# Optimization experiments

Hardware: AMD Instinct MI355X
Metric: run time of the kernel (lower is better)

The kernel has to match this reference:

```python
import jax, jax.numpy as jnp
import numpy as np

V, E, H, DV = 32000, 512, 1024, 512
B, K = 64, 49


def setup_inputs():
    key = jax.random.key(0)
    ks = jax.random.split(key, 16)
    p = lambda i, shape: jax.random.normal(ks[i], shape, dtype=jnp.float32) * 0.02
    return {
        "thought": jax.random.normal(ks[0], (B, H), dtype=jnp.float32),
        "visual_features": jax.random.normal(ks[1], (B, K, DV), dtype=jnp.float32),
        "max_len": 64,
        "embedding": p(2, (V, E)),
        "Wih1": p(3, (4 * H, E)), "Whh1": p(4, (4 * H, H)),
        "bih1": jnp.zeros((4 * H,), jnp.float32), "bhh1": jnp.zeros((4 * H,), jnp.float32),
        "Wih2": p(5, (4 * H, H)), "Whh2": p(6, (4 * H, H)),
        "bih2": jnp.zeros((4 * H,), jnp.float32), "bhh2": jnp.zeros((4 * H,), jnp.float32),
        "Wg1": p(7, (H, H)), "bg1": jnp.zeros((H,), jnp.float32),
        "Wg2": p(8, (1, H)), "bg2": jnp.zeros((1,), jnp.float32),
        "Wo": p(9, (V, H)), "bo": jnp.zeros((V,), jnp.float32),
        "Wv": p(10, (H, DV)), "bv": jnp.zeros((H,), jnp.float32),
        "ln_g": jnp.ones((H,), jnp.float32), "ln_b": jnp.zeros((H,), jnp.float32),
    }


def _lstm_cell(x, h, c, Wih, Whh, bih, bhh):
    # PyTorch LSTM gate order: i, f, g, o
    z = x @ Wih.T + h @ Whh.T + bih + bhh
    i, f, g, o = jnp.split(z, 4, axis=-1)
    c_new = jax.nn.sigmoid(f) * c + jax.nn.sigmoid(i) * jnp.tanh(g)
    h_new = jax.nn.sigmoid(o) * jnp.tanh(c_new)
    return h_new, c_new


def reference(thought, visual_features, max_len, embedding, Wih1, Whh1, bih1, bhh1,
              Wih2, Whh2, bih2, bbh2=None, bih2_dummy=None, **_unused):
    raise RuntimeError('placeholder')


def reference(thought, visual_features, max_len, embedding, Wih1, Whh1, bih1, bhh1,
              Wih2, Whh2, bih2, bhh2, Wg1, bg1, Wg2, bg2, Wo, bo, Wv, bv, ln_g, ln_b):
    Bsz, Hd = thought.shape
    temperature = 0.4  # epoch = 0 -> 0.4 + 0.4*0
    top_p = 0.7        # epoch = 0 -> 0.7 + 0.2*0
    scale = 1.0 / jnp.sqrt(jnp.asarray(Hd, jnp.float32))
    # visual_proj: Linear + LayerNorm (Dropout is identity in eval mode)
    vp = visual_features @ Wv.T + bv
    mu = vp.mean(-1, keepdims=True)
    var = vp.var(-1, keepdims=True)
    vp = (vp - mu) / jnp.sqrt(var + 1e-5) * ln_g + ln_b  # [B,K,H]
    b_idx = jnp.arange(Bsz)
    # carry: (h1,c1,h2,c2, input token, last-3 token history, history validity)
    init = (thought, jnp.zeros_like(thought), thought, jnp.zeros_like(thought),
            jnp.full((Bsz,), 1, jnp.int32),
            jnp.zeros((Bsz, 3), jnp.int32), jnp.zeros((Bsz, 3), jnp.bool_))
    keys = jax.random.split(jax.random.key(42), max_len)

    def step(carry, key):
        h1, c1, h2, c2, inp, hist, histv = carry
        emb = embedding[inp]  # [B,E]
        h1, c1 = _lstm_cell(emb, h1, c1, Wih1, Whh1, bih1, bhh1)
        h2, c2 = _lstm_cell(h1, h2, c2, Wih2, Whh2, bih2, bhh2)
        gate = jax.nn.sigmoid(jnp.tanh(h2 @ Wg1.T + bg1) @ Wg2.T + bg2)  # [B,1]
        out = h2 * gate
        attn = jax.nn.softmax(jnp.einsum('bh,bkh->bk', out, vp) * scale, axis=-1)
        out = out + jnp.einsum('bk,bkh->bh', attn, vp)
        logits = out @ Wo.T + bo  # [B,V]
        # repetition penalty: -2.0 once per UNIQUE token in last-3 history (set semantics via .max)
        pen = jnp.zeros_like(logits).at[b_idx[:, None], hist].max(histv.astype(logits.dtype))
        logits = (logits - 2.0 * pen) / temperature
        # nucleus (top-p) filtering, matching top_k_top_p_filtering with top_k=0
        order = jnp.argsort(-logits, axis=-1)
        sl = jnp.take_along_axis(logits, order, axis=-1)
        cum = jnp.cumsum(jax.nn.softmax(sl, axis=-1), axis=-1)
        rem = cum > top_p
        rem = jnp.concatenate([jnp.zeros_like(rem[:, :1]), rem[:, :-1]], axis=-1)
        mask = jnp.zeros_like(rem).at[b_idx[:, None], order].set(rem)
        logits = jnp.where(mask, -jnp.inf, logits)
        nxt = jax.random.categorical(key, logits).astype(jnp.int32)  # multinomial sample
        hist = jnp.concatenate([hist[:, 1:], nxt[:, None]], axis=1)
        histv = jnp.concatenate([histv[:, 1:], jnp.ones((Bsz, 1), jnp.bool_)], axis=1)
        return (h1, c1, h2, c2, nxt, hist, histv), nxt

    _, toks = jax.lax.scan(step, init, keys)
    return toks.T  # [B, max_len]
```

## Files before the change

### kernel.cpp

```cpp
#include <hip/hip_runtime.h>
#include <hip/hip_bf16.h>
#include <stdint.h>


#define B_   64
#define H_   1024
#define E_   512
#define DV_  512
#define KV_  49
#define V_   32000
#define T_   64

__device__ __forceinline__ uint32_t rotl32(uint32_t x, int r) {
  return (x << r) | (x >> (32 - r));
}
__device__ __forceinline__ void tf2x32(uint32_t k0, uint32_t k1,
                                       uint32_t x0, uint32_t x1,
                                       uint32_t& o0, uint32_t& o1) {
  uint32_t ks0 = k0, ks1 = k1, ks2 = k0 ^ k1 ^ 0x1BD11BDAu;
  x0 += ks0; x1 += ks1;
#define RND_(r) { x0 += x1; x1 = rotl32(x1, r) ^ x0; }
  RND_(13) RND_(15) RND_(26) RND_(6)  x0 += ks1; x1 += ks2 + 1u;
  RND_(17) RND_(29) RND_(16) RND_(24) x0 += ks2; x1 += ks0 + 2u;
  RND_(13) RND_(15) RND_(26) RND_(6)  x0 += ks0; x1 += ks1 + 3u;
  RND_(17) RND_(29) RND_(16) RND_(24) x0 += ks1; x1 += ks2 + 4u;
  RND_(13) RND_(15) RND_(26) RND_(6)  x0 += ks2; x1 += ks0 + 5u;
#undef RND_
  o0 = x0; o1 = x1;
}

__device__ __forceinline__ unsigned key_of(float f) {
  unsigned u = __float_as_uint(f);
  return (u & 0x80000000u) ? ~u : (u | 0x80000000u);
}
__device__ __forceinline__ float sigf(float x) { return 1.0f / (1.0f + expf(-x)); }

template <int BN, int TM, int TN, int NTHR>
__global__ __launch_bounds__(NTHR)
void gemm_dq(const float* __restrict__ A0, int lda0, const float* __restrict__ W0,
             int ldw0, int K0, float* __restrict__ out0, int ldo0, int nt0,
             const float* __restrict__ A1, int lda1, const float* __restrict__ W1,
             int ldw1, int K1, float* __restrict__ out1, int ldo1) {
  constexpr int LD = 36;
  constexpr int ROWS = 64 + BN;
  constexpr int NF4 = ROWS * 8 / NTHR;
  constexpr int BUFST = ROWS * LD;
  constexpr int CG = BN / TN;
  static_assert(ROWS * 8 % NTHR == 0, "staging divisibility");
  static_assert((64 / TM) * CG == NTHR, "thread grid");
  static_assert(TN == 4, "float4 epilogue");
  __shared__ __align__(16) float S[2][ROWS][LD];

  const int tid = threadIdx.x;
  const int bx = blockIdx.x;
  const float* A; const float* W; float* out;
  int lda, ldw, K, ldo, n0;
  if (bx < nt0) { A = A0; W = W0; out = out0; lda = lda0; ldw = ldw0; K = K0; ldo = ldo0; n0 = bx * BN; }
  else          { A = A1; W = W1; out = out1; lda = lda1; ldw = ldw1; K = K1; ldo = ldo1; n0 = (bx - nt0) * BN; }
  const int m0 = blockIdx.y * 64;
  const int tc = tid % CG, tr = tid / CG;

  const float* gp[NF4];
  float* lp[NF4];
#pragma unroll
  for (int q = 0; q < NF4; ++q) {
    int l = tid + q * NTHR;
    int r = l >> 3, c4 = l & 7;
    gp[q] = (l < 512) ? (A + (m0 + r) * lda + c4 * 4)
                      : (W + (n0 + (r - 64)) * ldw + c4 * 4);
    lp[q] = &S[0][r][(c4 ^ ((r >> 2) & 7)) << 2];
  }

  float4 pre[NF4];
#pragma unroll
  for (int q = 0; q < NF4; ++q) pre[q] = *(const float4*)gp[q];
#pragma unroll
  for (int q = 0; q < NF4; ++q) *(float4*)lp[q] = pre[q];
  __syncthreads();

  float acc[TM][TN] = {};
  const int nch = K >> 5;
  for (int c = 0; c < nch; ++c) {
    const bool more = (c + 1 < nch);
    if (more) {
      const int kc = (c + 1) << 5;
#pragma unroll
      for (int q = 0; q < NF4; ++q) pre[q] = *(const float4*)(gp[q] + kc);
    }
    const float* Sb = &S[c & 1][0][0];
#pragma unroll
    for (int kk = 0; kk < 8; ++kk) {
      float4 a4[TM], w4[TN];
#pragma unroll
      for (int i = 0; i < TM; ++i) {
        int m = tr * TM + i;
        a4[i] = *(const float4*)(Sb + m * LD + ((kk ^ ((m >> 2) & 7)) << 2));
      }
#pragma unroll
      for (int j = 0; j < TN; ++j) {
        int rw = 64 + tc * TN + j;
        w4[j] = *(const float4*)(Sb + rw * LD + ((kk ^ ((rw >> 2) & 7)) << 2));
      }
#pragma unroll
      for (int i = 0; i < TM; ++i)
#pragma unroll
        for (int j = 0; j < TN; ++j) {
          acc[i][j] = fmaf(a4[i].x, w4[j].x, acc[i][j]);
          acc[i][j] = fmaf(a4[i].y, w4[j].y, acc[i][j]);
          acc[i][j] = fmaf(a4[i].z, w4[j].z, acc[i][j]);
          acc[i][j] = fmaf(a4[i].w, w4[j].w, acc[i][j]);
        }
    }
    if (more) {
      const int bo2 = ((c + 1) & 1) * BUFST;
#pragma unroll
      for (int q = 0; q < NF4; ++q) *(float4*)(lp[q] + bo2) = pre[q];
    }
    __syncthreads();
  }

#pragma unroll
  for (int i = 0; i < TM; ++i) {
    float4 o;
    o.x = acc[i][0]; o.y = acc[i][1]; o.z = acc[i][2]; o.w = acc[i][3];
    *(float4*)&out[(m0 + tr * TM + i) * ldo + n0 + tc * TN] = o;
  }
}

__global__ __launch_bounds__(256)
void ln_vp(float* __restrict__ vp, const float* __restrict__ bv,
           const float* __restrict__ g, const float* __restrict__ bt) {
  int row = blockIdx.x, tid = threadIdx.x;
  __shared__ float buf[H_];
  __shared__ float red[256];
  float* p = vp + (long long)row * H_;
  for (int h = tid; h < H_; h += 256) buf[h] = __fadd_rn(p[h], bv[h]);
  __syncthreads();
  float s = 0;
  for (int h = tid; h < H_; h += 256) s += buf[h];
  red[tid] = s; __syncthreads();
  for (int off = 128; off > 0; off >>= 1) { if (tid < off) red[tid] += red[tid + off]; __syncthreads(); }
  float mu = red[0] / (float)H_;
  __syncthreads();
  float vs = 0;
  for (int h = tid; h < H_; h += 256) { float d = buf[h] - mu; vs += d * d; }
  red[tid] = vs; __syncthreads();
  for (int off = 128; off > 0; off >>= 1) { if (tid < off) red[tid] += red[tid + off]; __syncthreads(); }
  float var = red[0] / (float)H_;
  float sq = sqrtf(var + 1e-5f);
  for (int h = tid; h < H_; h += 256) {
    float nrm = __fdiv_rn(__fsub_rn(buf[h], mu), sq);
    p[h] = __fadd_rn(__fmul_rn(nrm, g[h]), bt[h]);
  }
}

__global__ __launch_bounds__(256)
void lstm_cell2(const float* __restrict__ dx, const float* __restrict__ dh,
                const float* __restrict__ bih, const float* __restrict__ bhh,
                float* __restrict__ c,
                float* __restrict__ hA, int ldA, float* __restrict__ hB, int ldB) {
  int idx = blockIdx.x * 256 + threadIdx.x;
  int b = idx >> 10, h = idx & 1023;
  float z[4];
#pragma unroll
  for (int g = 0; g < 4; g++) {
    int j = g * 1024 + h;
    float s = __fadd_rn(dx[b * 4096 + j], dh[b * 4096 + j]);
    s = __fadd_rn(s, bih[j]);
    s = __fadd_rn(s, bhh[j]);
    z[g] = s;
  }
  float fc = __fmul_rn(sigf(z[1]), c[idx]);
  float ig = __fmul_rn(sigf(z[0]), tanhf(z[2]));
  float cn = __fadd_rn(fc, ig);
  float hn = __fmul_rn(sigf(z[3]), tanhf(cn));
  c[idx] = cn;
  hA[(long long)b * ldA + h] = hn;
  hB[(long long)b * ldB + h] = hn;
}

__global__ __launch_bounds__(256)
void gate_attn_f(const float* __restrict__ WgT, const float* __restrict__ bg1,
                 const float* __restrict__ Wg2, const float* __restrict__ bg2,
                 const float* __restrict__ h2buf, const float* __restrict__ vp,
                 float* __restrict__ ctx) {
  int b = blockIdx.x, tid = threadIdx.x;
  __shared__ float t1[H_], outv[H_], attn[64];
  __shared__ float gate_s;
  {
    float s0 = 0, s1 = 0, s2 = 0, s3 = 0;
    for (int k = 0; k < H_; ++k) {
      float hk = h2buf[b * H_ + k];
      const float* wr = WgT + k * H_;
      s0 = fmaf(hk, wr[tid], s0);
      s1 = fmaf(hk, wr[tid + 256], s1);
      s2 = fmaf(hk, wr[tid + 512], s2);
      s3 = fmaf(hk, wr[tid + 768], s3);
    }
    t1[tid]       = tanhf(__fadd_rn(s0, bg1[tid]));
    t1[tid + 256] = tanhf(__fadd_rn(s1, bg1[tid + 256]));
    t1[tid + 512] = tanhf(__fadd_rn(s2, bg1[tid + 512]));
    t1[tid + 768] = tanhf(__fadd_rn(s3, bg1[tid + 768]));
  }
  __syncthreads();
  if (tid == 0) {
    float s = 0;
    for (int h = 0; h < H_; h++) s = fmaf(t1[h], Wg2[h], s);
    gate_s = sigf(__fadd_rn(s, bg2[0]));
  }
  __syncthreads();
  float gate = gate_s;
  for (int h = tid; h < H_; h += 256) outv[h] = __fmul_rn(h2buf[b * H_ + h], gate);
  __syncthreads();
  if (tid < KV_) {
    const float* vrow = vp + ((long long)b * KV_ + tid) * H_;
    float a = 0;
    for (int h = 0; h < H_; h++) a = fmaf(outv[h], vrow[h], a);
    attn[tid] = __fmul_rn(a, 0.03125f);
  }
  __syncthreads();
  if (tid == 0) {
    float m = -INFINITY;
    for (int k = 0; k < KV_; k++) m = fmaxf(m, attn[k]);
    float ss = 0;
    for (int k = 0; k < KV_; k++) { attn[k] = expf(attn[k] - m); ss += attn[k]; }
    for (int k = 0; k < KV_; k++) attn[k] = __fdiv_rn(attn[k], ss);
  }
  __syncthreads();
  for (int h = tid; h < H_; h += 256) {
    float acc = 0;
    for (int k = 0; k < KV_; k++) acc = fmaf(attn[k], vp[((long long)b * KV_ + k) * H_ + h], acc);
    ctx[b * H_ + h] = __fadd_rn(outv[h], acc);
  }
}

__global__ __launch_bounds__(256)
void init_state(const float* __restrict__ thought, const float* __restrict__ embedding,
                const float* __restrict__ Wg1, float* __restrict__ WgT,
                float* c1, float* c2, float* xcat1, float* xcat2,
                int* hist, int* histv) {
  int i = blockIdx.x * 256 + threadIdx.x;
  if (i < B_ * H_) {
    int b = i >> 10, h = i & 1023;
    c1[i] = 0.f; c2[i] = 0.f;
    float th = thought[i];
    xcat1[b * (E_ + H_) + E_ + h] = th;
    xcat2[b * (2 * H_) + H_ + h] = th;
    if (h < E_) xcat1[b * (E_ + H_) + h] = embedding[E_ + h];
  }
  if (i < B_ * 3) { hist[i] = 0; histv[i] = 0; }
  for (int x = i; x < H_ * H_; x += 256 * 256) {
    int k = x >> 10, j = x & 1023;
    WgT[x] = Wg1[j * H_ + k];
  }
}

__global__ __launch_bounds__(1024)
void sample_kernel(const float* __restrict__ dlog, const float* __restrict__ bo,
                   int* __restrict__ hist, int* __restrict__ histv,
                   const float* __restrict__ embedding, float* __restrict__ xcat1,
                   int* __restrict__ outTok, int t) {
  int b = blockIdx.x, tid = threadIdx.x;
  __shared__ float redf[1024];
  __shared__ int   redi[1024];
  __shared__ unsigned long long whist[8][257];
  __shared__ unsigned long long suf[256];
  __shared__ unsigned long long wq[4];
  __shared__ int jstar_s;
  __shared__ unsigned long long carry_s;
  __shared__ unsigned prefix_s;

  int hh0 = hist[b * 3 + 0], hh1 = hist[b * 3 + 1], hh2 = hist[b * 3 + 2];
  int p0 = histv[b * 3 + 0] ? hh0 : -1;
  int p1 = histv[b * 3 + 1] ? hh1 : -1;
  int p2 = histv[b * 3 + 2] ? hh2 : -1;
  const float* pa = dlog + (long long)b * V_;

  float L[32];
  float lm = -INFINITY;
#pragma unroll
  for (int e = 0; e < 32; ++e) {
    int v = tid + (e << 10);
    float l = -INFINITY;
    if (v < V_) {
      float raw = __fadd_rn(pa[v], bo[v]);
      if (v == p0 || v == p1 || v == p2) raw = __fsub_rn(raw, 2.0f);
      l = __fdiv_rn(raw, 0.4f);
      lm = fmaxf(lm, l);
    }
    L[e] = l;
  }
  redf[tid] = lm; __syncthreads();
  for (int off = 512; off > 0; off >>= 1) { if (tid < off) redf[tid] = fmaxf(redf[tid], redf[tid + off]); __syncthreads(); }
  float m = redf[0];
  __syncthreads();

  float ls = 0;
#pragma unroll
  for (int e = 0; e < 32; ++e) {
    int v = tid + (e << 10);
    if (v < V_) ls += expf(L[e] - m);
  }
  redf[tid] = ls; __syncthreads();
  for (int off = 512; off > 0; off >>= 1) { if (tid < off) redf[tid] += redf[tid + off]; __syncthreads(); }
  float Z = redf[0];
  __syncthreads();

  const double SC = 17592186044416.0;
  const unsigned long long B0 =
      (unsigned long long)(0.699999988079071044921875 * 17592186044416.0);
  if (tid == 0) { carry_s = 0ull; prefix_s = 0u; }
  __syncthreads();
  const int wid = tid >> 7;
  for (int pass = 0; pass < 4; pass++) {
    int shift = 24 - 8 * pass;
    unsigned maskk = (pass == 0) ? 0u : (0xFFFFFFFFu << (shift + 8));
    for (int i = tid; i < 8 * 257; i += 1024) ((unsigned long long*)whist)[i] = 0ull;
    __syncthreads();
    unsigned pref = prefix_s;
    unsigned long long carry = carry_s;
#pragma unroll
    for (int e = 0; e < 32; ++e) {
      int v = tid + (e << 10);
      if (v < V_) {
        unsigned key = key_of(L[e]);
        if ((key & maskk) == pref) {
          unsigned bin = (key >> shift) & 255u;
          float ee = expf(L[e] - m);
          unsigned long long S = (unsigned long long)((double)(ee / Z) * SC);
          atomicAdd(&whist[wid][bin], (S << 16) | 1ull);
        }
      }
    }
    __syncthreads();

    unsigned long long bs = 0ull;
    if (tid < 256) {
#pragma unroll
      for (int w = 0; w < 8; ++w) bs += whist[w][tid];
    }
    if (tid == 0) jstar_s = 256;
    __syncthreads();
    unsigned long long sown = 0ull, sincl = 0ull;
    if (tid < 256) {
      sown = bs >> 16;
      sincl = sown;
#pragma unroll
      for (int off = 1; off < 64; off <<= 1) {
        unsigned long long o = __shfl_down(sincl, off);
        if ((tid & 63) + off < 64) sincl += o;
      }
      if ((tid & 63) == 0) wq[tid >> 6] = sincl;
    }
    __syncthreads();
    if (tid < 256) {
      unsigned long long add = 0ull;
      for (int w2 = (tid >> 6) + 1; w2 < 4; ++w2) add += wq[w2];
      suf[tid] = sincl + add - sown;
    }
    __syncthreads();
    if (tid < 256 && (unsigned)(bs & 0xFFFFull) > 0u) {
      unsigned long long A = carry + suf[tid];
      if (A <= B0) atomicMin(&jstar_s, tid);
    }
    __syncthreads();
    if (tid == 0) {
      int j = jstar_s;
      carry_s = carry + suf[j];
      prefix_s = pref | (((unsigned)j) << shift);
    }
    __syncthreads();
  }
  unsigned Kstar = prefix_s;

  unsigned kt0, kt1;
  tf2x32(0u, 42u, 0u, (unsigned)t, kt0, kt1);

  float bestv = -INFINITY; int besti = 0x7fffffff;
#pragma unroll
  for (int e = 0; e < 32; ++e) {
    int v = tid + (e << 10);
    if (v < V_) {
      float l = L[e];
      if (key_of(l) >= Kstar) {
        unsigned r0, r1;
        tf2x32(kt0, kt1, 0u, (unsigned)(b * V_ + v), r0, r1);
        unsigned bits = r0 ^ r1;
        float u = __uint_as_float((bits >> 9) | 0x3f800000u) - 1.0f;
        u = fmaxf(u, 1.17549435e-38f);
        float gum = -logf(-logf(u));
        float val = __fadd_rn(l, gum);
        if (val > bestv) { bestv = val; besti = v; }
      }
    }
  }
  redf[tid] = bestv; redi[tid] = besti; __syncthreads();
  for (int off = 512; off > 0; off >>= 1) {
    if (tid < off) {
      float ov = redf[tid + off]; int oi = redi[tid + off];
      if (ov > redf[tid] || (ov == redf[tid] && oi < redi[tid])) { redf[tid] = ov; redi[tid] = oi; }
    }
    __syncthreads();
  }
  int tok = redi[0];
  if (tid == 0) {
    outTok[b * T_ + t] = tok;
    hist[b * 3 + 0] = hh1; hist[b * 3 + 1] = hh2; hist[b * 3 + 2] = tok;
    int v1 = histv[b * 3 + 1], v2 = histv[b * 3 + 2];
    histv[b * 3 + 0] = v1; histv[b * 3 + 1] = v2; histv[b * 3 + 2] = 1;
  }
  for (int k = tid; k < E_; k += 1024)
    xcat1[b * (E_ + H_) + k] = embedding[(long long)tok * E_ + k];
}

extern "C" void kernel_launch(void* const* d_in, const int* in_sizes, int n_in,
                              void* d_out, int out_size, void* d_ws, size_t ws_size,
                              hipStream_t stream) {
  const float* thought   = (const float*)d_in[0];
  const float* visf      = (const float*)d_in[1];
  const float* embedding = (const float*)d_in[3];
  const float* Wih1 = (const float*)d_in[4];
  const float* Whh1 = (const float*)d_in[5];
  const float* bih1 = (const float*)d_in[6];
  const float* bhh1 = (const float*)d_in[7];
  const float* Wih2 = (const float*)d_in[8];
  const float* Whh2 = (const float*)d_in[9];
  const float* bih2 = (const float*)d_in[10];
  const float* bhh2 = (const float*)d_in[11];
  const float* Wg1  = (const float*)d_in[12];
  const float* bg1  = (const float*)d_in[13];
  const float* Wg2  = (const float*)d_in[14];
  const float* bg2  = (const float*)d_in[15];
  const float* Wo   = (const float*)d_in[16];
  const float* bo   = (const float*)d_in[17];
  const float* Wv   = (const float*)d_in[18];
  const float* bv   = (const float*)d_in[19];
  const float* ln_g = (const float*)d_in[20];
  const float* ln_b = (const float*)d_in[21];
  int* outTok = (int*)d_out;

  float* ws = (float*)d_ws;
  long long off = 0;
  float* vp    = ws + off; off += (long long)B_ * KV_ * H_;
  float* xcat1 = ws + off; off += B_ * (E_ + H_);
  float* xcat2 = ws + off; off += B_ * (2 * H_);
  float* c1    = ws + off; off += B_ * H_;
  float* c2    = ws + off; off += B_ * H_;
  float* h2buf = ws + off; off += B_ * H_;
  float* ctx   = ws + off; off += B_ * H_;
  float* dx    = ws + off; off += (long long)B_ * 4096;
  float* dh    = ws + off; off += (long long)B_ * 4096;
  float* dlog  = ws + off; off += (long long)B_ * V_;
  float* WgT   = ws + off; off += (long long)H_ * H_;
  int* hist  = (int*)(ws + off); off += 256;
  int* histv = (int*)(ws + off); off += 256;

  init_state<<<256, 256, 0, stream>>>(thought, embedding, Wg1, WgT,
                                      c1, c2, xcat1, xcat2, hist, histv);

  gemm_dq<128, 8, 4, 256><<<dim3(8, KV_), 256, 0, stream>>>(
      visf, DV_, Wv, DV_, DV_, vp, H_, 8,
      visf, DV_, Wv, DV_, DV_, vp, H_);
  ln_vp<<<B_ * KV_, 256, 0, stream>>>(vp, bv, ln_g, ln_b);

  for (int t = 0; t < T_; t++) {
    gemm_dq<32, 4, 4, 128><<<dim3(256, 1), 128, 0, stream>>>(
        xcat1, E_ + H_, Wih1, E_, E_, dx, 4096, 128,
        xcat1 + E_, E_ + H_, Whh1, H_, H_, dh, 4096);
    lstm_cell2<<<256, 256, 0, stream>>>(dx, dh, bih1, bhh1, c1,
                                        xcat1 + E_, E_ + H_, xcat2, 2 * H_);
    gemm_dq<32, 4, 4, 128><<<dim3(256, 1), 128, 0, stream>>>(
        xcat2, 2 * H_, Wih2, H_, H_, dx, 4096, 128,
        xcat2 + H_, 2 * H_, Whh2, H_, H_, dh, 4096);
    lstm_cell2<<<256, 256, 0, stream>>>(dx, dh, bih2, bhh2, c2,
                                        h2buf, H_, xcat2 + H_, 2 * H_);
    gate_attn_f<<<B_, 256, 0, stream>>>(WgT, bg1, Wg2, bg2, h2buf, vp, ctx);
    gemm_dq<128, 8, 4, 256><<<dim3(250, 1), 256, 0, stream>>>(
        ctx, H_, Wo, H_, H_, dlog, V_, 250,
        ctx, H_, Wo, H_, H_, dlog, V_);
    sample_kernel<<<B_, 1024, 0, stream>>>(dlog, bo, hist, histv,
                                           embedding, xcat1, outTok, t);
  }
}
```

Baseline: 29.83 ms.

## Move gate projection to a parallel GEMM and retune GEMM tile configurations

The gate's first linear layer used to run inside gate_attn as a per-batch matvec over a transposed Wg1, with one 256-thread block per batch row. It now runs as a separate gemm_dq launch over 32 column tiles, so gate_attn only applies bias and tanh. The Wg1 transpose in init_state is removed. The LSTM GEMMs move to 256 threads with a smaller per-thread tile, and the output-logit GEMM moves to 64-wide tiles across 500 blocks. This spreads more blocks across CUs, at the cost of one extra kernel launch per step and possibly less register reuse per thread.

After: 29.98 ms. No clear change (+0.5%).

```diff
diff --git a/kernel.cpp b/kernel.cpp
--- a/kernel.cpp
+++ b/kernel.cpp
@@ -180,28 +180,15 @@
 }
 
 __global__ __launch_bounds__(256)
-void gate_attn_f(const float* __restrict__ WgT, const float* __restrict__ bg1,
-                 const float* __restrict__ Wg2, const float* __restrict__ bg2,
-                 const float* __restrict__ h2buf, const float* __restrict__ vp,
-                 float* __restrict__ ctx) {
+void gate_attn(const float* __restrict__ dg, const float* __restrict__ bg1,
+               const float* __restrict__ Wg2, const float* __restrict__ bg2,
+               const float* __restrict__ h2buf, const float* __restrict__ vp,
+               float* __restrict__ ctx) {
   int b = blockIdx.x, tid = threadIdx.x;
   __shared__ float t1[H_], outv[H_], attn[64];
   __shared__ float gate_s;
-  {
-    float s0 = 0, s1 = 0, s2 = 0, s3 = 0;
-    for (int k = 0; k < H_; ++k) {
-      float hk = h2buf[b * H_ + k];
-      const float* wr = WgT + k * H_;
-      s0 = fmaf(hk, wr[tid], s0);
-      s1 = fmaf(hk, wr[tid + 256], s1);
-      s2 = fmaf(hk, wr[tid + 512], s2);
-      s3 = fmaf(hk, wr[tid + 768], s3);
-    }
-    t1[tid]       = tanhf(__fadd_rn(s0, bg1[tid]));
-    t1[tid + 256] = tanhf(__fadd_rn(s1, bg1[tid + 256]));
-    t1[tid + 512] = tanhf(__fadd_rn(s2, bg1[tid + 512]));
-    t1[tid + 768] = tanhf(__fadd_rn(s3, bg1[tid + 768]));
-  }
+  for (int h = tid; h < H_; h += 256)
+    t1[h] = tanhf(__fadd_rn(dg[b * H_ + h], bg1[h]));
   __syncthreads();
   if (tid == 0) {
     float s = 0;
@@ -236,7 +223,6 @@
 
 __global__ __launch_bounds__(256)
 void init_state(const float* __restrict__ thought, const float* __restrict__ embedding,
-                const float* __restrict__ Wg1, float* __restrict__ WgT,
                 float* c1, float* c2, float* xcat1, float* xcat2,
                 int* hist, int* histv) {
   int i = blockIdx.x * 256 + threadIdx.x;
@@ -249,10 +235,6 @@
     if (h < E_) xcat1[b * (E_ + H_) + h] = embedding[E_ + h];
   }
   if (i < B_ * 3) { hist[i] = 0; histv[i] = 0; }
-  for (int x = i; x < H_ * H_; x += 256 * 256) {
-    int k = x >> 10, j = x & 1023;
-    WgT[x] = Wg1[j * H_ + k];
-  }
 }
 
 __global__ __launch_bounds__(1024)
@@ -450,13 +432,12 @@
   float* ctx   = ws + off; off += B_ * H_;
   float* dx    = ws + off; off += (long long)B_ * 4096;
   float* dh    = ws + off; off += (long long)B_ * 4096;
+  float* dg    = ws + off; off += (long long)B_ * H_;
   float* dlog  = ws + off; off += (long long)B_ * V_;
-  float* WgT   = ws + off; off += (long long)H_ * H_;
   int* hist  = (int*)(ws + off); off += 256;
   int* histv = (int*)(ws + off); off += 256;
 
-  init_state<<<256, 256, 0, stream>>>(thought, embedding, Wg1, WgT,
-                                      c1, c2, xcat1, xcat2, hist, histv);
+  init_state<<<256, 256, 0, stream>>>(thought, embedding, c1, c2, xcat1, xcat2, hist, histv);
 
   gemm_dq<128, 8, 4, 256><<<dim3(8, KV_), 256, 0, stream>>>(
       visf, DV_, Wv, DV_, DV_, vp, H_, 8,
@@ -464,19 +445,22 @@
   ln_vp<<<B_ * KV_, 256, 0, stream>>>(vp, bv, ln_g, ln_b);
 
   for (int t = 0; t < T_; t++) {
-    gemm_dq<32, 4, 4, 128><<<dim3(256, 1), 128, 0, stream>>>(
+    gemm_dq<32, 2, 4, 256><<<dim3(256, 1), 256, 0, stream>>>(
         xcat1, E_ + H_, Wih1, E_, E_, dx, 4096, 128,
         xcat1 + E_, E_ + H_, Whh1, H_, H_, dh, 4096);
     lstm_cell2<<<256, 256, 0, stream>>>(dx, dh, bih1, bhh1, c1,
                                         xcat1 + E_, E_ + H_, xcat2, 2 * H_);
-    gemm_dq<32, 4, 4, 128><<<dim3(256, 1), 128, 0, stream>>>(
+    gemm_dq<32, 2, 4, 256><<<dim3(256, 1), 256, 0, stream>>>(
         xcat2, 2 * H_, Wih2, H_, H_, dx, 4096, 128,
         xcat2 + H_, 2 * H_, Whh2, H_, H_, dh, 4096);
     lstm_cell2<<<256, 256, 0, stream>>>(dx, dh, bih2, bhh2, c2,
                                         h2buf, H_, xcat2 + H_, 2 * H_);
-    gate_attn_f<<<B_, 256, 0, stream>>>(WgT, bg1, Wg2, bg2, h2buf, vp, ctx);
-    gemm_dq<128, 8, 4, 256><<<dim3(250, 1), 256, 0, stream>>>(
-        ctx, H_, Wo, H_, H_, dlog, V_, 250,
+    gemm_dq<32, 2, 4, 256><<<dim3(32, 1), 256, 0, stream>>>(
+        h2buf, H_, Wg1, H_, H_, dg, H_, 32,
+        h2buf, H_, Wg1, H_, H_, dg, H_);
+    gate_attn<<<B_, 256, 0, stream>>>(dg, bg1, Wg2, bg2, h2buf, vp, ctx);
+    gemm_dq<64, 4, 4, 256><<<dim3(500, 1), 256, 0, stream>>>(
+        ctx, H_, Wo, H_, H_, dlog, V_, 500,
         ctx, H_, Wo, H_, H_, dlog, V_);
     sample_kernel<<<B_, 1024, 0, stream>>>(dlog, bo, hist, histv,
                                            embedding, xcat1, outTok, t);
```
